# Performance work log

Measured on AMD Instinct MI355X. Metric: run time of the kernel, lower is better.

## Reference

```python
import math
import jax, jax.numpy as jnp
import numpy as np

N, C, H, W = 8, 128, 112, 112
# frozen random.randint shifts from __init__
S7_01, S8_10 = 2, -1          # roll along dim1 (c), dim3 (h)
S11_11, S12_10, S12_11, S13_11 = 1, -1, 0, 1  # rolls along dim4 (w) / dim3 (h)


def _conv(x, w, padding, rhs_dilation=(1, 1), groups=1):
    return jax.lax.conv_general_dilated(
        x, w, window_strides=(1, 1), padding=padding,
        lhs_dilation=(1, 1), rhs_dilation=rhs_dilation,
        dimension_numbers=('NCHW', 'OIHW', 'NCHW'),
        feature_group_count=groups)


def setup_inputs() -> dict:
    key = jax.random.key(0)
    ks = jax.random.split(key, 6)
    x = jax.random.normal(ks[0], (N, C, H, W), jnp.float32)
    w3 = jax.random.normal(ks[1], (C, C, 1, 3), jnp.float32) * 0.02   # Conv2d(c,c,(1,3),dil=(1,2),pad=(0,2))
    w4 = jax.random.normal(ks[2], (C, 1, 7, 1), jnp.float32) * 0.02   # depthwise Conv2d(c,c,(7,1),dil=(3,1),pad=(9,0),groups=c)
    w9 = jax.random.normal(ks[3], (1, C, C), jnp.float32) * 0.02      # p_9_w
    w10 = jax.random.normal(ks[4], (1, C, 7, 1, 1), jnp.float32) * 0.02  # p_10_w
    w15 = jax.random.normal(ks[5], (C, C * 7 // 4, 1, 1), jnp.float32) * 0.02  # Conv2d(c*7,c,1,groups=4)
    return {"x": x, "w3": w3, "w4": w4, "w9": w9, "w10": w10, "w15": w15}


def reference(x, w3, w4, w9, w10, w15):
    n, c, h, w = x.shape
    hw = h * w
    t1 = jax.nn.sigmoid(x)
    t2 = t1 * x                                   # SiLU
    t3 = _conv(t2, w3, ((0, 0), (2, 2)), rhs_dilation=(1, 2))
    t4 = _conv(t3, w4, ((9, 9), (0, 0)), rhs_dilation=(3, 1), groups=c)
    # channel attention: bmm(t1, t0^T) / sqrt(h*w) -> (n,c,c)
    t5 = jnp.einsum('ncs,nds->ncd', t1.reshape(n, c, hw), x.reshape(n, c, hw)) / math.sqrt(hw)
    # F.unfold(t4, (7,1), dilation=(2,1), padding=(6,0)) -> (n,c,7,h,w)
    padded = jnp.pad(t4, ((0, 0), (0, 0), (6, 6), (0, 0)))
    t6 = jnp.stack([padded[:, :, 2 * k:2 * k + h, :] for k in range(7)], axis=2)
    t7 = jnp.roll(t6, S7_01, axis=1)
    t8 = jnp.roll(t7, S8_10, axis=3)
    t9 = w9 * t5
    t10 = w10 * t8
    t11 = jnp.roll(t10, S11_11, axis=4)
    t12 = jnp.roll(jnp.roll(t11, S12_10, axis=3), S12_11, axis=4)
    t13 = jnp.roll(t12, S13_11, axis=4)
    # bmm(t9^T, t2) / sqrt(c): out[n,d,s] = sum_c t9[n,c,d] * t2[n,c,s]
    t14 = (jnp.einsum('ncd,ncs->nds', t9, t2.reshape(n, c, hw)) / math.sqrt(c)).reshape(n, c, h, w)
    t15 = _conv(t13.reshape(n, c * 7, h, w), w15, ((0, 0), (0, 0)), groups=4)
    return t15 + t14
```

## Files before the change

kernel.cpp:

```cpp
#include <hip/hip_runtime.h>
#include <hip/hip_bf16.h>

#define NB 8
#define CC 128
#define HH 112
#define WW 112
#define HWS (HH*WW)
#define PLANE (CC*HWS)
#define TOT (NB*PLANE)
#define XP 116
#define LROW 130
#define PLANEP ((size_t)HH*XP*CC)
#define NSPLIT 49

typedef __attribute__((ext_vector_type(8))) short short8v;
typedef __attribute__((ext_vector_type(4))) float float4v;

__device__ __forceinline__ float bflo(unsigned u){ return __uint_as_float(u<<16); }
__device__ __forceinline__ float bfhi(unsigned u){ return __uint_as_float(u & 0xffff0000u); }
__device__ __forceinline__ float ldv(const float* p, size_t i){ return p[i]; }
__device__ __forceinline__ float ldv(const ushort* p, size_t i){ return __uint_as_float(((unsigned)p[i])<<16); }
__device__ __forceinline__ void ld8(const ushort* p, float* v){
    uint4 u0 = *((const uint4*)p);
    v[0]=bflo(u0.x); v[1]=bfhi(u0.x); v[2]=bflo(u0.y); v[3]=bfhi(u0.y);
    v[4]=bflo(u0.z); v[5]=bfhi(u0.z); v[6]=bflo(u0.w); v[7]=bfhi(u0.w);
}
__device__ __forceinline__ void ld8(const float* p, float* v){
    float4 a = *((const float4*)p); float4 b = *((const float4*)(p+4));
    v[0]=a.x; v[1]=a.y; v[2]=a.z; v[3]=a.w; v[4]=b.x; v[5]=b.y; v[6]=b.z; v[7]=b.w;
}
__device__ __forceinline__ void ld4(const float* p, float* v){
    float4 a = *((const float4*)p);
    v[0]=a.x; v[1]=a.y; v[2]=a.z; v[3]=a.w;
}
__device__ __forceinline__ void ld4(const ushort* p, float* v){
    uint2 u = *((const uint2*)p);
    v[0]=bflo(u.x); v[1]=bfhi(u.x); v[2]=bflo(u.y); v[3]=bfhi(u.y);
}
__device__ __forceinline__ ushort f2bf(float f){
    unsigned u = __float_as_uint(f);
    return (ushort)((u + 0x7fffu + ((u>>16)&1u)) >> 16);
}
__device__ __forceinline__ void stv(float* o, size_t i, float v){ o[i]=v; }
__device__ __forceinline__ void stv(ushort* o, size_t i, float v){ o[i]=f2bf(v); }
__device__ __forceinline__ float fsigmoid(float v){
    float e = __builtin_amdgcn_exp2f(v * -1.44269504f);
    return __builtin_amdgcn_rcpf(1.f + e);
}
__device__ __forceinline__ short8v ldbf(const ushort* p){ return *((const short8v*)p); }
__device__ __forceinline__ short8v ldbf(const float* p){
    float v[8]; ld8(p, v);
    ushort tmp[8];
    #pragma unroll
    for (int j=0;j<8;j++) tmp[j]=f2bf(v[j]);
    return *((const short8v*)tmp);
}

__global__ __launch_bounds__(256) void detect_k(const ushort* __restrict__ x, int* __restrict__ flag){
    __shared__ int cnt;
    if (threadIdx.x==0) cnt = 0;
    __syncthreads();
    int bad = 0;
    for (int i = threadIdx.x; i < 2048; i += 256){
        float v = ldv(x, i);
        if (!(v > -1e4f && v < 1e4f)) bad++;
    }
    atomicAdd(&cnt, bad);
    __syncthreads();
    if (threadIdx.x==0) *flag = (cnt > 64) ? 1 : 0;
}

template<typename ET>
__device__ __forceinline__ void wpack_body(const ET* __restrict__ w3, ushort* __restrict__ Wpk){
    int idx = blockIdx.x*256 + threadIdx.x;
    if (idx < CC*384){
        int o = idx/384, kap = idx - o*384;
        int k = kap>>7, i = kap&127;
        Wpk[idx] = f2bf(ldv(w3, (o*128+i)*3 + k));
    }
}
__global__ __launch_bounds__(256) void wpack_k(const void* w3, ushort* Wpk, const int* fl){
    if (*fl) wpack_body((const float*)w3, Wpk); else wpack_body((const ushort*)w3, Wpk);
}

template<typename ET>
__device__ __forceinline__ void bpad_body(const ET* __restrict__ x, ushort* __restrict__ Bpad){
    int y = blockIdx.x, n = blockIdx.y;
    __shared__ ushort px[XP*LROW];
    const ET* xb = x + (size_t)n*PLANE + y*WW;
    for (int idx=threadIdx.x; idx<CC*28; idx+=256){
        int i = idx/28, xq = (idx - i*28)*4;
        float v[4]; ld4(xb + (size_t)i*HWS + xq, v);
        #pragma unroll
        for (int d=0;d<4;d++){
            float vv = v[d];
            px[(xq+d+2)*LROW + i] = f2bf(vv * fsigmoid(vv));
        }
    }
    for (int idx=threadIdx.x; idx<4*CC; idx+=256){
        int j = idx >> 7, i = idx & 127;
        int xp = (j<2) ? j : j+112;
        px[xp*LROW + i] = 0;
    }
    __syncthreads();
    ushort* ob = Bpad + ((size_t)n*HH + y)*XP*CC;
    for (int idx=threadIdx.x; idx<XP*16; idx+=256){
        int xp = idx >> 4, c8 = idx & 15;
        const ushort* pr = px + xp*LROW + c8*8;
        uint4 v;
        v.x = *((const uint*)(pr+0));
        v.y = *((const uint*)(pr+2));
        v.z = *((const uint*)(pr+4));
        v.w = *((const uint*)(pr+6));
        *((uint4*)(ob + (size_t)xp*CC + c8*8)) = v;
    }
}
__global__ __launch_bounds__(256) void bpad_k(const void* x, ushort* Bpad, const int* fl){
    if (*fl) bpad_body((const float*)x, Bpad); else bpad_body((const ushort*)x, Bpad);
}

__global__ __launch_bounds__(256) void conv3mm_k(const ushort* __restrict__ Bpad, const ushort* __restrict__ Wpk,
                                                 ushort* __restrict__ t3T){
    int bx = blockIdx.x;
    int n  = blockIdx.y;
    int sbi = bx >> 1, oh = bx & 1;
    int wid = threadIdx.x >> 6, lane = threadIdx.x & 63;
    int l15 = lane & 15, quad = lane >> 4;
    __shared__ ushort Alds[24576];
    {
        const int tid = threadIdx.x;
        uint4 tmp[12];
        #pragma unroll
        for (int it=0; it<12; it++){
            int g = it*256 + tid;
            int kcmt = g >> 6, sl = (g>>2)&15, sq = g&3;
            int kc = kcmt >> 2, mt = kcmt & 3;
            tmp[it] = *((const uint4*)(Wpk + (size_t)(oh*64 + mt*16 + sl)*384 + kc*32 + sq*8));
        }
        #pragma unroll
        for (int it=0; it<12; it++){
            int g = it*256 + tid;
            *((uint4*)(Alds + g*8)) = tmp[it];
        }
    }
    __syncthreads();

    int s0 = sbi*128 + wid*32;
    int s1 = s0 + l15, s2 = s1 + 16;
    int y1 = s1/WW, x1 = s1 - y1*WW;
    int y2 = s2/WW, x2 = s2 - y2*WW;
    const ushort* bb = Bpad + (size_t)n*PLANEP;
    const ushort* b1p = bb + ((size_t)y1*XP + x1)*CC + quad*8;
    const ushort* b2p = bb + ((size_t)y2*XP + x2)*CC + quad*8;
    const ushort* al = Alds + l15*32 + quad*8;

    float4v acc[4][2] = {};
    short8v BA[2][4], BB[2][4], a0[4], a1[4];

    auto ldb = [&](int g, short8v (&B)[2][4]){
        #pragma unroll
        for (int m=0;m<4;m++){
            B[0][m] = *((const short8v*)(b1p + g*256 + m*32));
            B[1][m] = *((const short8v*)(b2p + g*256 + m*32));
        }
    };
    auto lda = [&](int kc, short8v (&dst)[4]){
        #pragma unroll
        for (int mt=0;mt<4;mt++) dst[mt] = *((const short8v*)(al + (kc*4+mt)*512));
    };
    auto step = [&](const short8v (&a)[4], const short8v (&B)[2][4], int m){
        #pragma unroll
        for (int mt=0;mt<4;mt++){
            acc[mt][0] = __builtin_amdgcn_mfma_f32_16x16x32_bf16(a[mt], B[0][m], acc[mt][0],0,0,0);
            acc[mt][1] = __builtin_amdgcn_mfma_f32_16x16x32_bf16(a[mt], B[1][m], acc[mt][1],0,0,0);
        }
    };

    ldb(0, BA); lda(0, a0);
    ldb(1, BB);
    lda(1, a1);  step(a0, BA, 0);
    lda(2, a0);  step(a1, BA, 1);
    lda(3, a1);  step(a0, BA, 2);
    lda(4, a0);  step(a1, BA, 3);
    ldb(2, BA);
    lda(5, a1);  step(a0, BB, 0);
    lda(6, a0);  step(a1, BB, 1);
    lda(7, a1);  step(a0, BB, 2);
    lda(8, a0);  step(a1, BB, 3);
    lda(9, a1);  step(a0, BA, 0);
    lda(10, a0); step(a1, BA, 1);
    lda(11, a1); step(a0, BA, 2);
                 step(a1, BA, 3);

    ushort* tb = t3T + (size_t)n*PLANE;
    #pragma unroll
    for (int nt=0; nt<2; nt++){
        int s = s0 + nt*16 + l15;
        ushort* rowp = tb + (size_t)s*128 + oh*64 + quad*4;
        #pragma unroll
        for (int mt=0; mt<4; mt++){
            ushort4 v;
            v.x = f2bf(acc[mt][nt][0]); v.y = f2bf(acc[mt][nt][1]);
            v.z = f2bf(acc[mt][nt][2]); v.w = f2bf(acc[mt][nt][3]);
            *((ushort4*)(rowp + mt*16)) = v;
        }
    }
}

template<typename ET>
__device__ __forceinline__ void wdpack_body(const ET* __restrict__ w4, float* __restrict__ wdp){
    int idx = blockIdx.x*256 + threadIdx.x;
    if (idx < 896){ int k = idx >> 7, c = idx & 127; wdp[idx] = ldv(w4, c*7 + k); }
}
__global__ __launch_bounds__(256) void wdpack_k(const void* w4, float* wdp, const int* fl){
    if (*fl) wdpack_body((const float*)w4, wdp); else wdpack_body((const ushort*)w4, wdp);
}

__global__ __launch_bounds__(256) void dwconvT_k(const ushort* __restrict__ t3T, const float* __restrict__ wdp,
                                                 ushort* __restrict__ t4T){
    int by = blockIdx.x, n = blockIdx.y;
    int y = (by>>3) + (by&7)*14;
    const ushort* tb = t3T + (size_t)n*PLANE;
    ushort* ob = t4T + (size_t)n*PLANE + (size_t)y*WW*128;
    for (int it = threadIdx.x; it < WW*16; it += 256){
        int c8 = it & 15, x = it >> 4;
        int coff = c8*8;
        float acc8[8] = {0.f,0.f,0.f,0.f,0.f,0.f,0.f,0.f};
        #pragma unroll
        for (int k=0;k<7;k++){
            int row = y - 9 + 3*k;
            if (row < 0 || row >= HH) continue;
            float v[8]; ld8(tb + ((size_t)row*WW + x)*128 + coff, v);
            const float* wp = wdp + k*128 + coff;
            #pragma unroll
            for (int j=0;j<8;j++) acc8[j] = fmaf(wp[j], v[j], acc8[j]);
        }
        ushort tmp[8];
        #pragma unroll
        for (int j=0;j<8;j++) tmp[j] = f2bf(acc8[j]);
        *((short8v*)(ob + (size_t)x*128 + coff)) = *((const short8v*)tmp);
    }
}

template<typename ET>
__device__ __forceinline__ void fusew_body(const ET* __restrict__ w10, const ET* __restrict__ w15,
                                           ushort* __restrict__ Wfb){
    int idx = blockIdx.x*256+threadIdx.x;
    if (idx < CC*224){
        int o = idx / 224, r = idx - o*224;
        int g = o >> 5;
        int cl = r/7, k = r - cl*7;
        int c = g*32 + cl;
        Wfb[idx] = f2bf(ldv(w15, o*224 + r) * ldv(w10, c*7+k));
    }
}
__global__ __launch_bounds__(256) void fusew_k(const void* w10, const void* w15, ushort* Wfb, const int* fl){
    if (*fl) fusew_body((const float*)w10, (const float*)w15, Wfb);
    else     fusew_body((const ushort*)w10, (const ushort*)w15, Wfb);
}

__global__ __launch_bounds__(256) void wfapack_k(const ushort* __restrict__ Wfb, ushort* __restrict__ Wfa){
    int idx = blockIdx.x*256 + threadIdx.x;
    if (idx >= 57344) return;
    int j   = idx & 31;
    int l15 = (idx >> 5) & 15;
    int mt  = (idx >> 9) & 1;
    int q   = (idx >> 10) & 1;
    int k   = (idx >> 11) % 7;
    int w   = idx / 14336;
    int o = w*32 + mt*16 + l15;
    int cl = -1;
    if (q==1){ if (j < 30) cl = j + 2; }
    else     { if (j >= 30) cl = j - 30; }
    Wfa[idx] = (cl >= 0) ? Wfb[o*224 + cl*7 + k] : (ushort)0;
}

template<int ST0, int NST>
__device__ __forceinline__ void t15_body_v6(const ushort* __restrict__ tbase, const ushort* __restrict__ Wfa,
                                            ushort* __restrict__ urow, int y, int w, int l15, int quad,
                                            ushort* lds){
    int qlo = (w+3)&3;
    int tid = threadIdx.x;
    float4v acc[NST][2] = {};
    int klo = (y >= 6) ? 0 : ((7 - y) >> 1);
    int khi = min(6, (117 - y) >> 1);
    int nk = khi - klo;

    const int swz = (tid>>4)&7;
    const int wbase = tid & ~63;

    auto dma_row = [&](int k, int bufi){
        const ushort* rs = tbase + ((size_t)(y + 2*k - 6)*WW + ST0*16)*128;
        #pragma unroll
        for (int j=0;j<NST;j++){
            int g  = j*256 + tid;
            int gs = g ^ swz;
            const ushort* gp = rs + (size_t)gs*8;
            ushort* lp = lds + (size_t)bufi*8192 + (size_t)(j*256 + wbase)*8;
            __builtin_amdgcn_global_load_lds((const __attribute__((address_space(1))) void*)gp,
                                             (__attribute__((address_space(3))) void*)lp, 16, 0, 0);
        }
    };
    auto issueA = [&](int k, short8v (&A)[4]){
        const ushort* af = Wfa + (w*7 + k)*2048 + l15*32 + quad*8;
        A[0] = *((const short8v*)(af));
        A[1] = *((const short8v*)(af + 512));
        A[2] = *((const short8v*)(af + 1024));
        A[3] = *((const short8v*)(af + 1536));
    };
    auto domm = [&](int bufi, const short8v (&A)[4]){
        const ushort* lb = lds + bufi*8192;
        #pragma unroll
        for (int st=0; st<NST; st++){
            int xl = st*16 + l15;
            int g0 = xl*16 + qlo*4 + quad;  g0 ^= (g0>>4)&7;
            int g1 = xl*16 + w*4   + quad;  g1 ^= (g1>>4)&7;
            short8v B0 = *((const short8v*)(lb + g0*8));
            short8v B1 = *((const short8v*)(lb + g1*8));
            acc[st][0] = __builtin_amdgcn_mfma_f32_16x16x32_bf16(A[0], B0, acc[st][0], 0,0,0);
            acc[st][1] = __builtin_amdgcn_mfma_f32_16x16x32_bf16(A[1], B0, acc[st][1], 0,0,0);
            acc[st][0] = __builtin_amdgcn_mfma_f32_16x16x32_bf16(A[2], B1, acc[st][0], 0,0,0);
            acc[st][1] = __builtin_amdgcn_mfma_f32_16x16x32_bf16(A[3], B1, acc[st][1], 0,0,0);
        }
    };
    auto iter = [&](int i, short8v (&Acur)[4], short8v (&Anx)[4]){
        if (i+2 <= nk){
            if constexpr (NST==4) asm volatile("s_waitcnt vmcnt(8)" ::: "memory");
            else                  asm volatile("s_waitcnt vmcnt(7)" ::: "memory");
        } else {
            asm volatile("s_waitcnt vmcnt(0)" ::: "memory");
        }
        __builtin_amdgcn_s_barrier();
        __builtin_amdgcn_sched_barrier(0);
        if (i+1 <= nk) issueA(klo+i+1, Anx);
        if (i+2 <= nk) dma_row(klo+i+2, (i+2)%3);
        domm(i%3, Acur);
    };

    short8v A0[4], A1[4];
    dma_row(klo,   0);
    dma_row(klo+1, 1);
    issueA(klo, A0);

    for (int i=0; i<=nk; i+=2){
        iter(i, A0, A1);
        if (i+1 <= nk) iter(i+1, A1, A0);
    }

    #pragma unroll
    for (int st=0; st<NST; st++){
        int s = (ST0 + st)*16 + l15;
        ushort* p = urow + (size_t)s*128 + w*32 + quad*4;
        #pragma unroll
        for (int mt=0; mt<2; mt++){
            ushort4 v;
            v.x = f2bf(acc[st][mt][0]); v.y = f2bf(acc[st][mt][1]);
            v.z = f2bf(acc[st][mt][2]); v.w = f2bf(acc[st][mt][3]);
            *((ushort4*)(p + mt*16)) = v;
        }
    }
}
__global__ __launch_bounds__(256) void t15v6_k(const ushort* __restrict__ t4T, const ushort* __restrict__ Wfa,
                                               ushort* __restrict__ uT){
    __shared__ ushort lds[3*8192];
    int bx = blockIdx.x, n = blockIdx.y;
    int xh = bx & 1, byi = bx >> 1;
    int y = (byi>>3) + (byi&7)*14;
    int w = threadIdx.x >> 6, lane = threadIdx.x & 63;
    int l15 = lane & 15, quad = lane >> 4;
    const ushort* tbase = t4T + (size_t)n*PLANE;
    ushort* urow = uT + (size_t)n*PLANE + (size_t)y*WW*128;
    if (xh == 0) t15_body_v6<0,4>(tbase, Wfa, urow, y, w, l15, quad, lds);
    else         t15_body_v6<4,3>(tbase, Wfa, urow, y, w, l15, quad, lds);
}

template<typename ET>
__device__ __forceinline__ void t5mm_body(const ET* __restrict__ x, float* __restrict__ t5part){
    int ks = blockIdx.x, n = blockIdx.y;
    int wid = threadIdx.x>>6, lane = threadIdx.x&63;
    int l15 = lane&15, quad = lane>>4;
    const ET* xn = x + (size_t)n*PLANE;
    float4v acc[2][8] = {};
    for (int t=0; t<8; t++){
        int sb = ks*256 + t*32 + quad*8;
        short8v afr[2];
        #pragma unroll
        for (int mt=0; mt<2; mt++){
            int row = wid*32 + mt*16 + l15;
            float v[8]; ld8(xn + (size_t)row*HWS + sb, v);
            ushort tmp[8];
            #pragma unroll
            for (int j=0;j<8;j++) tmp[j] = f2bf(fsigmoid(v[j]));
            afr[mt] = *((const short8v*)tmp);
        }
        #pragma unroll
        for (int nt=0; nt<8; nt++){
            int row = nt*16 + l15;
            short8v bfr = ldbf(xn + (size_t)row*HWS + sb);
            acc[0][nt] = __builtin_amdgcn_mfma_f32_16x16x32_bf16(afr[0], bfr, acc[0][nt], 0,0,0);
            acc[1][nt] = __builtin_amdgcn_mfma_f32_16x16x32_bf16(afr[1], bfr, acc[1][nt], 0,0,0);
        }
    }
    float* outp = t5part + (size_t)ks*(NB*16384) + (size_t)n*16384;
    #pragma unroll
    for (int mt=0; mt<2; mt++){
        #pragma unroll
        for (int nt=0; nt<8; nt++){
            #pragma unroll
            for (int r=0; r<4; r++){
                int ci = wid*32 + mt*16 + quad*4 + r;
                int cj = nt*16 + l15;
                outp[ci*128 + cj] = acc[mt][nt][r];
            }
        }
    }
}
__global__ __launch_bounds__(256) void t5mm_k(const void* x, float* t5part, const int* fl){
    if (*fl) t5mm_body((const float*)x, t5part); else t5mm_body((const ushort*)x, t5part);
}

template<typename ET>
__device__ __forceinline__ void coefb_body(const ET* __restrict__ w9, const float* __restrict__ t5part,
                                           ushort* __restrict__ coefb){
    const float sc = 7.89181775e-4f;
    int idx = blockIdx.x*256 + threadIdx.x;
    int n = idx >> 14, rem = idx & 16383;
    int c = rem >> 7, d = rem & 127;
    const float* p = t5part + (size_t)n*16384 + rem;
    float s = 0.f;
    #pragma unroll 7
    for (int ks=0; ks<NSPLIT; ks++) s += p[(size_t)ks*(NB*16384)];
    coefb[n*16384 + d*128 + c] = f2bf(ldv(w9, c*128 + d) * s * sc);
}
__global__ __launch_bounds__(256) void coefb_k(const void* w9, const float* t5part, ushort* coefb, const int* fl){
    if (*fl) coefb_body((const float*)w9, t5part, coefb); else coefb_body((const ushort*)w9, t5part, coefb);
}

template<typename OT>
__device__ __forceinline__ void final2_body(const ushort* __restrict__ Bpad, const ushort* __restrict__ coefb,
                                            const ushort* __restrict__ uT, OT* __restrict__ out){
    int sb = blockIdx.x, n = blockIdx.y;
    int wid = threadIdx.x>>6, lane = threadIdx.x&63;
    int l15 = lane&15, quad = lane>>4;
    int shalf = wid >> 1, ohalf = wid & 1;
    int s0 = sb*64 + shalf*32;
    int s1 = s0 + l15, s2 = s1 + 16;
    int y1 = s1/WW, x1 = s1 - y1*WW;
    int y2 = s2/WW, x2 = s2 - y2*WW;
    const ushort* bb = Bpad + (size_t)n*PLANEP;
    const ushort* b1p = bb + ((size_t)y1*XP + x1 + 2)*CC + quad*8;
    const ushort* b2p = bb + ((size_t)y2*XP + x2 + 2)*CC + quad*8;
    const ushort* abase = coefb + (size_t)n*16384 + (size_t)(ohalf*64 + l15)*128 + quad*8;
    float4v acc[4][2] = {};
    short8v bv0[4], bv1[4], aP[4], aQ[4];
    #pragma unroll
    for (int kc=0;kc<4;kc++){
        bv0[kc] = *((const short8v*)(b1p + kc*32));
        bv1[kc] = *((const short8v*)(b2p + kc*32));
    }
    auto lda = [&](int kc, short8v (&dst)[4]){
        #pragma unroll
        for (int mt=0;mt<4;mt++) dst[mt] = *((const short8v*)(abase + mt*16*128 + kc*32));
    };
    auto step = [&](const short8v (&a)[4], int kc){
        #pragma unroll
        for (int mt=0;mt<4;mt++){
            acc[mt][0] = __builtin_amdgcn_mfma_f32_16x16x32_bf16(a[mt], bv0[kc], acc[mt][0],0,0,0);
            acc[mt][1] = __builtin_amdgcn_mfma_f32_16x16x32_bf16(a[mt], bv1[kc], acc[mt][1],0,0,0);
        }
    };
    lda(0, aP);
    lda(1, aQ); step(aP, 0);
    lda(2, aP); step(aQ, 1);
    lda(3, aQ); step(aP, 2);
                step(aQ, 3);
    const ushort* uTn = uT + (size_t)n*PLANE;
    #pragma unroll
    for (int nt=0; nt<2; nt++){
        int s = s0 + nt*16 + l15;
        int y = s/WW, xx = s - y*WW;
        int ys = y+2; if (ys>=HH) ys-=HH;
        int xs = xx-2; if (xs<0) xs+=WW;
        const ushort* up = uTn + ((size_t)ys*WW + xs)*128 + ohalf*64 + quad*4;
        #pragma unroll
        for (int mt=0; mt<4; mt++){
            uint2 uv = *((const uint2*)(up + mt*16));
            float v0 = bflo(uv.x), vv1 = bfhi(uv.x), v2 = bflo(uv.y), v3 = bfhi(uv.y);
            int d = ohalf*64 + mt*16 + quad*4;
            stv(out, ((size_t)n*CC+d+0)*HWS + s, v0  + acc[mt][nt][0]);
            stv(out, ((size_t)n*CC+d+1)*HWS + s, vv1 + acc[mt][nt][1]);
            stv(out, ((size_t)n*CC+d+2)*HWS + s, v2  + acc[mt][nt][2]);
            stv(out, ((size_t)n*CC+d+3)*HWS + s, v3  + acc[mt][nt][3]);
        }
    }
}
__global__ __launch_bounds__(256) void final2_k(const ushort* Bpad, const ushort* coefb,
                                                const ushort* uT, void* out, const int* fl){
    if (*fl) final2_body(Bpad, coefb, uT, (float*)out);
    else     final2_body(Bpad, coefb, uT, (ushort*)out);
}

extern "C" void kernel_launch(void* const* d_in, const int* in_sizes, int n_in,
                              void* d_out, int out_size, void* d_ws, size_t ws_size,
                              hipStream_t stream) {
    const void* x   = d_in[0];
    const void* w3  = d_in[1];
    const void* w4  = d_in[2];
    const void* w9  = d_in[3];
    const void* w10 = d_in[4];
    const void* w15 = d_in[5];

    ushort* t3T  = (ushort*)d_ws;
    float*  t5part = (float*)t3T;
    ushort* uT   = t3T;
    ushort* t4T  = t3T + TOT;
    ushort* Bpad = t4T + TOT;
    ushort* coefb= (ushort*)(Bpad + NB*PLANEP);
    ushort* Wfb  = coefb + NB*CC*CC;
    ushort* Wpk  = Wfb + CC*224;
    ushort* Wfa  = Wpk + CC*384;
    float*  wdp  = (float*)(Wfa + 57344);
    int* flag    = (int*)(wdp + 896);

    detect_k<<<1, 256, 0, stream>>>((const ushort*)x, flag);

    wpack_k  <<<192, 256, 0, stream>>>(w3, Wpk, flag);
    fusew_k  <<<112, 256, 0, stream>>>(w10, w15, Wfb, flag);
    wfapack_k<<<224, 256, 0, stream>>>(Wfb, Wfa);
    wdpack_k <<<4,   256, 0, stream>>>(w4, wdp, flag);
    bpad_k   <<<dim3(HH,NB), 256, 0, stream>>>(x, Bpad, flag);
    conv3mm_k<<<dim3(196,NB), 256, 0, stream>>>(Bpad, Wpk, t3T);
    dwconvT_k<<<dim3(HH,NB), 256, 0, stream>>>(t3T, wdp, t4T);
    t5mm_k   <<<dim3(NSPLIT,NB), 256, 0, stream>>>(x, t5part, flag);
    coefb_k  <<<NB*CC*CC/256, 256, 0, stream>>>(w9, t5part, coefb, flag);
    t15v6_k  <<<dim3(224,NB), 256, 0, stream>>>(t4T, Wfa, uT);
    final2_k <<<dim3(196,NB), 256, 0, stream>>>(Bpad, coefb, uT, d_out, flag);
}
```

Before: 290.2 us.

## Stage t5 channel-attention GEMM through async LDS DMA and tighten conv waitcnt

For bf16 input, the t5 (sigmoid(x)·x^T) kernel now loads 32-column slabs of all 128 channels into a triple-buffered LDS ring with global_load_lds, using an XOR swizzle. Both MFMA operands are then read from LDS, so each x element is fetched once per block instead of twice from global memory, and loads overlap with compute. The conv pipeline's vmcnt waits are loosened to allow one fewer outstanding stage, and the bpad shared buffer is moved to kernel scope. The new waitcnt values have to match the number of loads in flight. If they do not, reads could race with the DMA.

```diff
diff --git a/kernel.cpp b/kernel.cpp
--- a/kernel.cpp
+++ b/kernel.cpp
@@ -84,9 +84,8 @@
 }
 
 template<typename ET>
-__device__ __forceinline__ void bpad_body(const ET* __restrict__ x, ushort* __restrict__ Bpad){
+__device__ __forceinline__ void bpad_body(const ET* __restrict__ x, ushort* __restrict__ Bpad, ushort* px){
     int y = blockIdx.x, n = blockIdx.y;
-    __shared__ ushort px[XP*LROW];
     const ET* xb = x + (size_t)n*PLANE + y*WW;
     for (int idx=threadIdx.x; idx<CC*28; idx+=256){
         int i = idx/28, xq = (idx - i*28)*4;
@@ -116,7 +115,8 @@
     }
 }
 __global__ __launch_bounds__(256) void bpad_k(const void* x, ushort* Bpad, const int* fl){
-    if (*fl) bpad_body((const float*)x, Bpad); else bpad_body((const ushort*)x, Bpad);
+    __shared__ ushort px[XP*LROW];
+    if (*fl) bpad_body((const float*)x, Bpad, px); else bpad_body((const ushort*)x, Bpad, px);
 }
 
 __global__ __launch_bounds__(256) void conv3mm_k(const ushort* __restrict__ Bpad, const ushort* __restrict__ Wpk,
@@ -324,9 +324,9 @@
         }
     };
     auto iter = [&](int i, short8v (&Acur)[4], short8v (&Anx)[4]){
-        if (i+2 <= nk){
-            if constexpr (NST==4) asm volatile("s_waitcnt vmcnt(8)" ::: "memory");
-            else                  asm volatile("s_waitcnt vmcnt(7)" ::: "memory");
+        if (i+1 <= nk){
+            if constexpr (NST==4) asm volatile("s_waitcnt vmcnt(4)" ::: "memory");
+            else                  asm volatile("s_waitcnt vmcnt(3)" ::: "memory");
         } else {
             asm volatile("s_waitcnt vmcnt(0)" ::: "memory");
         }
@@ -374,12 +374,86 @@
     else         t15_body_v6<4,3>(tbase, Wfa, urow, y, w, l15, quad, lds);
 }
 
-template<typename ET>
-__device__ __forceinline__ void t5mm_body(const ET* __restrict__ x, float* __restrict__ t5part){
+__device__ __forceinline__ void t5mm_dma_body(const ushort* __restrict__ x, float* __restrict__ t5part,
+                                              ushort* lds){
+    int ks = blockIdx.x, n = blockIdx.y;
+    int tid = threadIdx.x;
+    int wid = tid>>6, lane = tid&63;
+    int l15 = lane&15, quad = lane>>4;
+    const ushort* xn = x + (size_t)n*PLANE;
+    const int sb0 = ks*256;
+    const int wbase = tid & ~63;
+    float4v acc[2][8] = {};
+
+    auto dma = [&](int t, int bufi){
+        #pragma unroll
+        for (int j=0;j<2;j++){
+            int g  = j*256 + tid;
+            int ch = g>>2;
+            int pp = (g&3) ^ ((g>>3)&3);
+            const ushort* gp = xn + (size_t)ch*HWS + sb0 + t*32 + pp*8;
+            ushort* lp = lds + (size_t)bufi*4096 + (size_t)(j*256 + wbase)*8;
+            __builtin_amdgcn_global_load_lds((const __attribute__((address_space(1))) void*)gp,
+                                             (__attribute__((address_space(3))) void*)lp, 16, 0, 0);
+        }
+    };
+    auto domm = [&](int bufi){
+        const ushort* lb = lds + bufi*4096;
+        short8v afr[2];
+        #pragma unroll
+        for (int mt=0; mt<2; mt++){
+            int row = wid*32 + mt*16 + l15;
+            int g = row*4 + (quad ^ ((row>>1)&3));
+            uint4 u = *((const uint4*)(lb + g*8));
+            float v[8];
+            v[0]=bflo(u.x); v[1]=bfhi(u.x); v[2]=bflo(u.y); v[3]=bfhi(u.y);
+            v[4]=bflo(u.z); v[5]=bfhi(u.z); v[6]=bflo(u.w); v[7]=bfhi(u.w);
+            ushort tmp[8];
+            #pragma unroll
+            for (int j=0;j<8;j++) tmp[j] = f2bf(fsigmoid(v[j]));
+            afr[mt] = *((const short8v*)tmp);
+        }
+        #pragma unroll
+        for (int nt=0; nt<8; nt++){
+            int row = nt*16 + l15;
+            int g = row*4 + (quad ^ ((row>>1)&3));
+            short8v bfr = *((const short8v*)(lb + g*8));
+            acc[0][nt] = __builtin_amdgcn_mfma_f32_16x16x32_bf16(afr[0], bfr, acc[0][nt], 0,0,0);
+            acc[1][nt] = __builtin_amdgcn_mfma_f32_16x16x32_bf16(afr[1], bfr, acc[1][nt], 0,0,0);
+        }
+    };
+
+    dma(0, 0);
+    dma(1, 1);
+    #pragma unroll
+    for (int i=0; i<8; i++){
+        if (i < 7) asm volatile("s_waitcnt vmcnt(2)" ::: "memory");
+        else       asm volatile("s_waitcnt vmcnt(0)" ::: "memory");
+        __builtin_amdgcn_s_barrier();
+        __builtin_amdgcn_sched_barrier(0);
+        if (i+2 <= 7) dma(i+2, (i+2)%3);
+        domm(i%3);
+    }
+
+    float* outp = t5part + (size_t)ks*(NB*16384) + (size_t)n*16384;
+    #pragma unroll
+    for (int mt=0; mt<2; mt++){
+        #pragma unroll
+        for (int nt=0; nt<8; nt++){
+            #pragma unroll
+            for (int r=0; r<4; r++){
+                int ci = wid*32 + mt*16 + quad*4 + r;
+                int cj = nt*16 + l15;
+                outp[ci*128 + cj] = acc[mt][nt][r];
+            }
+        }
+    }
+}
+__device__ __forceinline__ void t5mm_f32_body(const float* __restrict__ x, float* __restrict__ t5part){
     int ks = blockIdx.x, n = blockIdx.y;
     int wid = threadIdx.x>>6, lane = threadIdx.x&63;
     int l15 = lane&15, quad = lane>>4;
-    const ET* xn = x + (size_t)n*PLANE;
+    const float* xn = x + (size_t)n*PLANE;
     float4v acc[2][8] = {};
     for (int t=0; t<8; t++){
         int sb = ks*256 + t*32 + quad*8;
@@ -416,7 +490,9 @@
     }
 }
 __global__ __launch_bounds__(256) void t5mm_k(const void* x, float* t5part, const int* fl){
-    if (*fl) t5mm_body((const float*)x, t5part); else t5mm_body((const ushort*)x, t5part);
+    __shared__ ushort lds[3*4096];
+    if (*fl) t5mm_f32_body((const float*)x, t5part);
+    else     t5mm_dma_body((const ushort*)x, t5part, lds);
 }
 
 template<typename ET>
```

Measured after the change: 281.6 us. 3.0% less time.
